# Optimization experiments

Measured on AMD Instinct MI355X. Metric: run time of the kernel, lower is better.

## Reference

```python
import jax, jax.numpy as jnp
from jax import lax
import numpy as np

H = 2048           # dec_units == encoder sequence length
LEAK = 0.2
EPS = 1e-5

def _leaky(x):
    return jnp.where(x >= 0, x, LEAK * x)

def _bn(x, g, b):
    # training-mode BatchNorm1d over (N, C, L): normalize per-channel over N and L
    m = x.mean(axis=(0, 2), keepdims=True)
    v = x.var(axis=(0, 2), keepdims=True)
    return (x - m) / jnp.sqrt(v + EPS) * g.reshape(1, -1, 1) + b.reshape(1, -1, 1)

def _conv(x, w, b):
    # x: (N, C, L), w: (O, I, K) -- valid conv, stride 1
    y = lax.conv_general_dilated(x, w, (1,), 'VALID', dimension_numbers=('NCH', 'OIH', 'NCH'))
    return y + b[None, :, None]

def setup_inputs() -> dict:
    key = jax.random.key(0)
    ks = jax.random.split(key, 40)
    def n(k, shape, s=0.05):
        return jax.random.normal(k, shape, dtype=jnp.float32) * s
    Lp = ((H - 20) // 2 - 8) // 2          # 503: conv/pool-reduced length
    inp = {
        'last_input': n(ks[0], (4,), 1.0),
        'hidden':     n(ks[1], (1, 1, H), 1.0),
        'enc_output': n(ks[2], (H, 1, 6), 1.0),
        'W1_w': n(ks[3], (H, 6)),   'W1_b': n(ks[4], (H,)),
        'W2_w': n(ks[5], (H, H)),   'W2_b': n(ks[6], (H,)),
        'V_w':  n(ks[7], (1, H + 1)), 'V_b': n(ks[8], (1,)),
        'bn1_g': 1.0 + n(ks[9], (1,)), 'bn1_b': n(ks[10], (1,)),
        'c1_w': n(ks[11], (6, 6, 11), 0.2), 'c1_b': n(ks[12], (6,)),
        'c2_w': n(ks[13], (6, 6, 11), 0.2), 'c2_b': n(ks[14], (6,)),
        'c3_w': n(ks[15], (6, 6, 5), 0.2),  'c3_b': n(ks[16], (6,)),
        'c4_w': n(ks[17], (6, 6, 5), 0.2),  'c4_b': n(ks[18], (6,)),
        'bn2_g': 1.0 + n(ks[19], (6,)), 'bn2_b': n(ks[20], (6,)),
        'gru_Wi': n(ks[21], (3 * H, 6), 0.2), 'gru_Wh': n(ks[22], (3 * H, H), 0.02),
        'gru_bi': n(ks[23], (3 * H,)),        'gru_bh': n(ks[24], (3 * H,)),
        'lin1_w': n(ks[25], (400, H), 0.02), 'lin1_b': n(ks[26], (400,)),
        'bn3_g': 1.0 + n(ks[27], (1,)), 'bn3_b': n(ks[28], (1,)),
        'lin2_w': n(ks[29], (1, 400)), 'lin2_b': n(ks[30], (1,)),
        'lin3_w': n(ks[31], (50, Lp + 4)), 'lin3_b': n(ks[32], (50,)),
        'lin4_w': n(ks[33], (4, 50)), 'lin4_b': n(ks[34], (4,)),
    }
    return inp

def _forward(last_input, hidden, enc_output, W1_w, W1_b, W2_w, W2_b, V_w, V_b,
             bn1_g, bn1_b, c1_w, c1_b, c2_w, c2_b, c3_w, c3_b, c4_w, c4_b,
             bn2_g, bn2_b, gru_Wi, gru_Wh, gru_bi, gru_bh,
             lin1_w, lin1_b, bn3_g, bn3_b, lin2_w, lin2_b, lin3_w, lin3_b, lin4_w, lin4_b):
    # --- Bahdanau-style attention score ---
    w1 = _leaky(enc_output @ W1_w.T + W1_b)                         # (H, 1, H)
    w2 = _leaky(jnp.transpose(hidden @ W2_w.T + W2_b, (2, 1, 0)))   # (H, 1, 1)
    cat = jnp.concatenate([w1, jnp.broadcast_to(w2, (H, 1, 1))], axis=-1)
    score = cat @ V_w.T + V_b                                       # (H, 1, 1)
    score = _leaky(_bn(score, bn1_g, bn1_b))
    weights = jax.nn.softmax(score, axis=0)
    context = jnp.transpose(enc_output * weights, (1, 2, 0))        # (1, 6, H)
    # --- small CNN feature extractor ---
    c = _leaky(_conv(context, c1_w, c1_b))
    c = _leaky(_conv(c, c2_w, c2_b))
    c = c.reshape(1, 6, -1, 2).max(axis=-1)                         # MaxPool1d(2)
    c = _leaky(_conv(c, c3_w, c3_b))
    c = _leaky(_conv(c, c4_w, c4_b))
    c = _bn(c, bn2_g, bn2_b)
    c = c.reshape(1, 6, -1, 2).max(axis=-1)                         # (1, 6, L')
    seq = jnp.transpose(c, (2, 0, 1))                               # (L', 1, 6)
    # --- GRU (torch gate order r, z, n) ---
    h0 = hidden[0]                                                  # (1, H)
    def step(h, x):
        gi = x @ gru_Wi.T + gru_bi
        gh = h @ gru_Wh.T + gru_bh
        ir, iz, inn = jnp.split(gi, 3, axis=-1)
        hr, hz, hn = jnp.split(gh, 3, axis=-1)
        r = jax.nn.sigmoid(ir + hr)
        z = jax.nn.sigmoid(iz + hz)
        ng = jnp.tanh(inn + r * hn)
        hn_new = (1.0 - z) * ng + z * h
        return hn_new, hn_new
    hT, xs = lax.scan(step, h0, seq)                                # xs: (L', 1, H)
    # --- MLP head (dropout = identity in eval) ---
    x = _leaky(xs)
    x = x @ lin1_w.T + lin1_b                                       # (L', 1, 400)
    x = _leaky(_bn(x, bn3_g, bn3_b))
    x = (x @ lin2_w.T + lin2_b).squeeze()                           # (L',)
    x = _leaky(x)
    x = jnp.concatenate([x, last_input])                            # (L'+4,)
    x = _leaky(x @ lin3_w.T + lin3_b)
    x = x @ lin4_w.T + lin4_b                                       # (4,)
    return x, hT[None]                                              # hidden: (1, 1, H)

def reference(last_input, hidden, enc_output, W1_w, W1_b, W2_w, W2_b, V_w, V_b,
              bn1_g, bn1_b, c1_w, c1_b, c2_w, c2_b, c3_w, c3_b, c4_w, c4_b,
              bn2_g, bn2_b, gru_Wi, gru_Wh, gru_bi, gru_bh,
              lin1_w, lin1_b, bn3_g, bn3_b, lin2_w, lin2_b, lin3_w, lin3_b, lin4_w, lin4_b):
    return _forward(last_input, hidden, enc_output, W1_w, W1_b, W2_w, W2_b, V_w, V_b,
                    bn1_g, bn1_b, c1_w, c1_b, c2_w, c2_b, c3_w, c3_b, c4_w, c4_b,
                    bn2_g, bn2_b, gru_Wi, gru_Wh, gru_bi, gru_bh,
                    lin1_w, lin1_b, bn3_g, bn3_b, lin2_w, lin2_b, lin3_w, lin3_b, lin4_w, lin4_b)
```

## Files before the change

### kernel.cpp

```cpp
#include <hip/hip_runtime.h>

#define LEAK 0.2f
#define EPS  1e-5f
#define TS   503
#define SCOPE_SYS __HIP_MEMORY_SCOPE_SYSTEM
typedef unsigned long long ull;

__device__ __forceinline__ float lrelu(float x){ return x >= 0.f ? x : LEAK * x; }

typedef _Float16 half2v __attribute__((ext_vector_type(2)));

__device__ __forceinline__ unsigned short f2h(float x){
  _Float16 h = (_Float16)x;
  return __builtin_bit_cast(unsigned short, h);
}

__device__ __forceinline__ float fdot2(unsigned a, unsigned b, float c){
#if __has_builtin(__builtin_amdgcn_fdot2)
  return __builtin_amdgcn_fdot2(__builtin_bit_cast(half2v, a),
                                __builtin_bit_cast(half2v, b), c, false);
#else
  half2v aa = __builtin_bit_cast(half2v, a);
  half2v bb = __builtin_bit_cast(half2v, b);
  return fmaf((float)aa[1], (float)bb[1], fmaf((float)aa[0], (float)bb[0], c));
#endif
}

template<bool MAXOP>
__device__ __forceinline__ float bred(float v, float* red){
  #pragma unroll
  for (int off = 32; off; off >>= 1){
    float o = __shfl_xor(v, off);
    v = MAXOP ? fmaxf(v, o) : (v + o);
  }
  int nw = blockDim.x >> 6;
  int wv = threadIdx.x >> 6, ln = threadIdx.x & 63;
  __syncthreads();
  if (ln == 0) red[wv] = v;
  __syncthreads();
  if (wv == 0){
    float x = (ln < nw) ? red[ln] : (MAXOP ? -3.402823466e38f : 0.f);
    #pragma unroll
    for (int off = 8; off; off >>= 1){
      float o = __shfl_xor(x, off);
      x = MAXOP ? fmaxf(x, o) : (x + o);
    }
    if (ln == 0) red[0] = x;
  }
  __syncthreads();
  return red[0];
}

__global__ void k_w2(const float* __restrict__ W2w, const float* __restrict__ W2b,
                     const float* __restrict__ hidden, float* __restrict__ w2v){
  int wave = threadIdx.x >> 6, lane = threadIdx.x & 63;
  int row = blockIdx.x*4 + wave;
  const float* wr = W2w + (size_t)row*2048;
  float acc = 0.f;
  #pragma unroll
  for (int k = 0; k < 8; ++k){
    int base = 4*lane + 256*k;
    float4 w = *(const float4*)(wr + base);
    float4 h = *(const float4*)(hidden + base);
    acc = fmaf(w.x,h.x, fmaf(w.y,h.y, fmaf(w.z,h.z, fmaf(w.w,h.w, acc))));
  }
  #pragma unroll
  for (int off = 32; off; off >>= 1) acc += __shfl_xor(acc, off);
  if (lane == 0) w2v[row] = lrelu(acc + W2b[row]);
}

__global__ void k_score(const float* __restrict__ enc, const float* __restrict__ W1w,
                        const float* __restrict__ W1b, const float* __restrict__ Vw,
                        const float* __restrict__ Vb, const float* __restrict__ w2v,
                        float* __restrict__ score){
  __shared__ float sW1[2048*6];
  int tid = threadIdx.x;
  for (int idx = tid; idx < 2048*6; idx += 256) sW1[idx] = W1w[idx];
  __syncthreads();
  int wave = tid >> 6, lane = tid & 63;
  int i = blockIdx.x*4 + wave;
  float e0 = enc[(size_t)i*6+0], e1 = enc[(size_t)i*6+1], e2 = enc[(size_t)i*6+2];
  float e3 = enc[(size_t)i*6+3], e4 = enc[(size_t)i*6+4], e5 = enc[(size_t)i*6+5];
  float acc = 0.f;
  for (int jj = 0; jj < 32; ++jj){
    int j = lane + 64*jj;
    const float* wr = sW1 + j*6;
    float a = fmaf(e0,wr[0], fmaf(e1,wr[1], fmaf(e2,wr[2],
              fmaf(e3,wr[3], fmaf(e4,wr[4], fmaf(e5,wr[5], W1b[j]))))));
    acc = fmaf(lrelu(a), Vw[j], acc);
  }
  #pragma unroll
  for (int off = 32; off; off >>= 1) acc += __shfl_xor(acc, off);
  if (lane == 0) score[i] = acc + w2v[i]*Vw[2048] + Vb[0];
}

__global__ void k_softctx(const float* __restrict__ enc, const float* __restrict__ score,
                          const float* g1, const float* b1, float* __restrict__ ctx){
  __shared__ float red[16];
  int tid = threadIdx.x;
  float s0 = score[tid], s1 = score[tid + 1024];
  float mean = bred<false>(s0 + s1, red) * (1.f/2048.f);
  float d0 = s0 - mean, d1 = s1 - mean;
  float var = bred<false>(d0*d0 + d1*d1, red) * (1.f/2048.f);
  float iv = rsqrtf(var + EPS);
  float g = g1[0], b = b1[0];
  float v0 = lrelu(d0*iv*g + b), v1 = lrelu(d1*iv*g + b);
  float mx = bred<true>(fmaxf(v0, v1), red);
  float e0 = expf(v0 - mx), e1 = expf(v1 - mx);
  float se = bred<false>(e0 + e1, red);
  float w0 = e0/se, w1 = e1/se;
  #pragma unroll
  for (int c = 0; c < 6; ++c){
    ctx[c*2048 + tid]        = enc[(size_t)tid*6 + c] * w0;
    ctx[c*2048 + tid + 1024] = enc[(size_t)(tid+1024)*6 + c] * w1;
  }
}

__global__ void k_conv(const float* __restrict__ in, int Lin,
                       float* __restrict__ out, int Lout,
                       const float* __restrict__ w, const float* __restrict__ b, int K){
  int idx = blockIdx.x*256 + threadIdx.x;
  if (idx >= 6*Lout) return;
  int o = idx / Lout, x = idx - o*Lout;
  float acc = b[o];
  for (int i = 0; i < 6; ++i){
    const float* ir = in + i*Lin + x;
    const float* wr = w + (o*6 + i)*K;
    for (int k = 0; k < K; ++k) acc = fmaf(ir[k], wr[k], acc);
  }
  out[o*Lout + x] = lrelu(acc);
}

__global__ void k_pool(const float* __restrict__ in, int Lin, float* __restrict__ out, int Lout){
  int idx = blockIdx.x*256 + threadIdx.x;
  if (idx >= 6*Lout) return;
  int o = idx / Lout, x = idx - o*Lout;
  out[idx] = fmaxf(in[o*Lin + 2*x], in[o*Lin + 2*x + 1]);
}

__global__ void k_bn2stats(const float* __restrict__ in, float* m6, float* i6){
  __shared__ float red[16];
  for (int c = 0; c < 6; ++c){
    float s = 0.f, s2 = 0.f;
    for (int i = threadIdx.x; i < 1006; i += 256){
      float v = in[c*1006 + i]; s += v; s2 += v*v;
    }
    s  = bred<false>(s, red);
    s2 = bred<false>(s2, red);
    if (threadIdx.x == 0){
      float m = s / 1006.f;
      float var = s2 / 1006.f - m*m;
      m6[c] = m; i6[c] = rsqrtf(var + EPS);
    }
  }
}

__global__ void k_seq(const float* __restrict__ cb4, const float* m6, const float* i6,
                      const float* g2, const float* b2, float* __restrict__ seq){
  int idx = blockIdx.x*256 + threadIdx.x;
  if (idx >= TS*6) return;
  int c = idx % 6, t = idx / 6;
  float m = m6[c], iv = i6[c], g = g2[c], b = b2[c];
  float v0 = (cb4[c*1006 + 2*t]     - m)*iv*g + b;
  float v1 = (cb4[c*1006 + 2*t + 1] - m)*iv*g + b;
  seq[idx] = fmaxf(v0, v1);
}

__global__ void k_gihat(const float* __restrict__ seq, const float* __restrict__ Wi,
                        const float* __restrict__ bi, float* __restrict__ gihat){
  int row = blockIdx.x*256 + threadIdx.x;
  int t = blockIdx.y;
  const float* s = seq + t*6;
  const float* w = Wi + (size_t)row*6;
  float v = fmaf(s[0],w[0], fmaf(s[1],w[1], fmaf(s[2],w[2],
            fmaf(s[3],w[3], fmaf(s[4],w[4], fmaf(s[5],w[5], bi[row]))))));
  gihat[(size_t)t*6144 + row] = v;
}

#define GRU_SMEM (24*2048*2 + 1024*4)

__global__ void __launch_bounds__(256, 1)
k_gru(const float* __restrict__ Wh, const float* __restrict__ bh,
      const float* __restrict__ hidden, const float* __restrict__ gihat,
      ull* hbuf, float* __restrict__ xs, float* __restrict__ dout){
  extern __shared__ char smem[];
  ushort* Wl    = (ushort*)smem;
  unsigned* h2  = (unsigned*)(smem + 24*2048*2);
  const int tid = threadIdx.x, wg = blockIdx.x;
  const int lane = tid & 63, w = tid >> 6;
  const int hbase = wg << 3;

  for (int idx = tid; idx < 24*2048; idx += 256){
    int lr = idx >> 11, col = idx & 2047;
    int wv = lr/6, k = lr - 6*wv, gate = k >> 1, o = k & 1;
    int grow = (gate << 11) + hbase + 2*wv + o;
    Wl[idx] = f2h(Wh[(size_t)grow*2048 + col]);
  }
  float bhr = 0.f, bhz = 0.f, bhn = 0.f, hold = 0.f;
  if (lane < 2){
    int o = hbase + 2*w + lane;
    bhr = bh[o]; bhz = bh[2048 + o]; bhn = bh[4096 + o];
    hold = hidden[o];
  }
  __syncthreads();

  for (int t = 0; t < TS; ++t){
    float gr = 0.f, gz = 0.f, gn = 0.f;
    if (lane < 2){
      const float* gp = gihat + (size_t)t*6144 + hbase + 2*w + lane;
      gr = gp[0]; gz = gp[2048]; gn = gp[4096];
    }
    if (t == 0){
      const float4* hp = (const float4*)(hidden + 8*tid);
      float4 a = hp[0], b = hp[1];
      unsigned p0 = (unsigned)f2h(a.x) | ((unsigned)f2h(a.y) << 16);
      unsigned p1 = (unsigned)f2h(a.z) | ((unsigned)f2h(a.w) << 16);
      unsigned p2 = (unsigned)f2h(b.x) | ((unsigned)f2h(b.y) << 16);
      unsigned p3 = (unsigned)f2h(b.z) | ((unsigned)f2h(b.w) << 16);
      *(uint4*)(h2 + 4*tid) = make_uint4(p0, p1, p2, p3);
    } else {
      const ull* src = hbuf + (size_t)((t - 1) & 1)*1024 + 4*tid;
      const unsigned expect = (unsigned)t;
      ull v[4];
      unsigned done = 0;
      for (;;){
        #pragma unroll
        for (int j = 0; j < 4; ++j)
          if (!((done >> j) & 1u))
            v[j] = __hip_atomic_load(src + j, __ATOMIC_RELAXED, SCOPE_SYS);
        unsigned nd = done;
        #pragma unroll
        for (int j = 0; j < 4; ++j)
          if ((unsigned)(v[j] >> 32) == expect) nd |= (1u << j);
        if (nd == 15u) break;
        done = nd;
        __builtin_amdgcn_s_sleep(1);
      }
      *(uint4*)(h2 + 4*tid) = make_uint4((unsigned)v[0], (unsigned)v[1],
                                         (unsigned)v[2], (unsigned)v[3]);
    }
    __syncthreads();

    uint4 hf[4];
    #pragma unroll
    for (int k = 0; k < 4; ++k)
      hf[k] = *(const uint4*)((const char*)h2 + 16*lane + 1024*k);
    float acc[6];
    #pragma unroll
    for (int rr = 0; rr < 6; ++rr){
      int lr = 6*w + rr;
      const char* wrow = (const char*)Wl + lr*4096 + 16*lane;
      float a = 0.f;
      #pragma unroll
      for (int k = 0; k < 4; ++k){
        uint4 wv = *(const uint4*)(wrow + 1024*k);
        a = fdot2(wv.x, hf[k].x, a);
        a = fdot2(wv.y, hf[k].y, a);
        a = fdot2(wv.z, hf[k].z, a);
        a = fdot2(wv.w, hf[k].w, a);
      }
      #pragma unroll
      for (int off = 32; off; off >>= 1) a += __shfl_xor(a, off);
      acc[rr] = a;
    }
    float hnew = 0.f;
    if (lane < 2){
      float r  = 1.f/(1.f + expf(-(gr + bhr + acc[0 + lane])));
      float z  = 1.f/(1.f + expf(-(gz + bhz + acc[2 + lane])));
      float ng = tanhf(gn + r*(acc[4 + lane] + bhn));
      hnew = (1.f - z)*ng + z*hold;
    }
    float hn1 = __shfl(hnew, 1);
    if (lane == 0){
      unsigned pair = (unsigned)f2h(hnew) | ((unsigned)f2h(hn1) << 16);
      ull pv = ((ull)(unsigned)(t + 1) << 32) | (ull)pair;
      __hip_atomic_store(hbuf + (size_t)(t & 1)*1024 + 4*wg + w, pv,
                         __ATOMIC_RELAXED, SCOPE_SYS);
    }
    if (lane < 2){
      xs[(size_t)t*2048 + hbase + 2*w + lane] = hnew;
      if (t == TS - 1) dout[4 + hbase + 2*w + lane] = hnew;
      hold = hnew;
    }
  }
}

__global__ void k_lin1(const float* __restrict__ xs, const float* __restrict__ W,
                       const float* __restrict__ B, float* __restrict__ y1){
  __shared__ float xT[32][36];
  __shared__ float wT[32][36];
  int tid = threadIdx.x;
  int m0 = blockIdx.y*32, n0 = blockIdx.x*32;
  int lm = tid >> 3, lk = (tid & 7)*4;
  int tx = tid & 15, ty = tid >> 4;
  float acc00=0.f, acc01=0.f, acc10=0.f, acc11=0.f;
  for (int k0 = 0; k0 < 2048; k0 += 32){
    float4 xv = make_float4(0.f,0.f,0.f,0.f);
    int tt = m0 + lm;
    if (tt < TS) xv = *(const float4*)(xs + (size_t)tt*2048 + k0 + lk);
    xT[lk+0][lm] = lrelu(xv.x); xT[lk+1][lm] = lrelu(xv.y);
    xT[lk+2][lm] = lrelu(xv.z); xT[lk+3][lm] = lrelu(xv.w);
    float4 wv = make_float4(0.f,0.f,0.f,0.f);
    int jj = n0 + lm;
    if (jj < 400) wv = *(const float4*)(W + (size_t)jj*2048 + k0 + lk);
    wT[lk+0][lm] = wv.x; wT[lk+1][lm] = wv.y; wT[lk+2][lm] = wv.z; wT[lk+3][lm] = wv.w;
    __syncthreads();
    #pragma unroll
    for (int k = 0; k < 32; ++k){
      float2 a = *(const float2*)&xT[k][2*ty];
      float2 b = *(const float2*)&wT[k][2*tx];
      acc00 = fmaf(a.x, b.x, acc00); acc01 = fmaf(a.x, b.y, acc01);
      acc10 = fmaf(a.y, b.x, acc10); acc11 = fmaf(a.y, b.y, acc11);
    }
    __syncthreads();
  }
  int t0 = m0 + 2*ty, j0 = n0 + 2*tx;
  if (t0 < TS){
    if (j0 < 400)   y1[t0*400 + j0]   = acc00 + B[j0];
    if (j0+1 < 400) y1[t0*400 + j0+1] = acc01 + B[j0+1];
  }
  if (t0+1 < TS){
    if (j0 < 400)   y1[(t0+1)*400 + j0]   = acc10 + B[j0];
    if (j0+1 < 400) y1[(t0+1)*400 + j0+1] = acc11 + B[j0+1];
  }
}

__global__ void k_bn3p(const float* __restrict__ y1, float* __restrict__ part){
  __shared__ float red[16];
  float s = 0.f, s2 = 0.f;
  for (int idx = blockIdx.x*256 + threadIdx.x; idx < TS*400; idx += 64*256){
    float v = y1[idx]; s += v; s2 += v*v;
  }
  s  = bred<false>(s, red);
  s2 = bred<false>(s2, red);
  if (threadIdx.x == 0){ part[blockIdx.x] = s; part[64 + blockIdx.x] = s2; }
}

__global__ void k_bn3f(const float* __restrict__ part, float* __restrict__ stats){
  int ln = threadIdx.x;
  float s = part[ln], s2 = part[64 + ln];
  #pragma unroll
  for (int off = 32; off; off >>= 1){ s += __shfl_xor(s, off); s2 += __shfl_xor(s2, off); }
  if (ln == 0){
    float m = s / (float)(TS*400);
    float var = s2 / (float)(TS*400) - m*m;
    stats[0] = m; stats[1] = rsqrtf(var + EPS);
  }
}

__global__ void k_x2(const float* __restrict__ y1, const float* __restrict__ stats,
                     const float* g3, const float* b3, const float* __restrict__ l2w,
                     const float* l2b, float* __restrict__ x2){
  int t = blockIdx.x, ln = threadIdx.x;
  float m = stats[0], iv = stats[1], g = g3[0], b = b3[0];
  float acc = 0.f;
  for (int j = ln; j < 400; j += 64)
    acc = fmaf(lrelu((y1[t*400 + j] - m)*iv*g + b), l2w[j], acc);
  #pragma unroll
  for (int off = 32; off; off >>= 1) acc += __shfl_xor(acc, off);
  if (ln == 0) x2[t] = lrelu(acc + l2b[0]);
}

__global__ void k_head(const float* __restrict__ x2, const float* __restrict__ last,
                       const float* __restrict__ l3w, const float* __restrict__ l3b,
                       const float* __restrict__ l4w, const float* __restrict__ l4b,
                       float* __restrict__ out){
  __shared__ float o1[50];
  int tid = threadIdx.x;
  if (tid < 50){
    float acc = l3b[tid];
    const float* wr = l3w + tid*507;
    for (int i = 0; i < TS; ++i) acc = fmaf(x2[i], wr[i], acc);
    for (int i = 0; i < 4; ++i)  acc = fmaf(last[i], wr[TS + i], acc);
    o1[tid] = lrelu(acc);
  }
  __syncthreads();
  if (tid < 4){
    float acc = l4b[tid];
    const float* wr = l4w + tid*50;
    for (int k = 0; k < 50; ++k) acc = fmaf(o1[k], wr[k], acc);
    out[tid] = acc;
  }
}

#define OFF_BN2M    1024u
#define OFF_BN2I    1056u
#define OFF_BN3P    2048u
#define OFF_BN3S    2560u
#define OFF_W2      4096u
#define OFF_SCORE   12288u
#define OFF_X2      20480u
#define OFF_CTX     24576u
#define OFF_CB1     73728u
#define OFF_HBUF    73728u
#define OFF_CB2     122880u
#define OFF_CP1     172032u
#define OFF_CB3     196608u
#define OFF_CB4     221184u
#define OFF_SEQ     245760u
#define OFF_GIHAT   274432u
#define OFF_XS      12636160u
#define OFF_Y1      16756736u

extern "C" void kernel_launch(void* const* d_in, const int* in_sizes, int n_in,
                              void* d_out, int out_size, void* d_ws, size_t ws_size,
                              hipStream_t stream){
  const float* last   = (const float*)d_in[0];
  const float* hidden = (const float*)d_in[1];
  const float* enc    = (const float*)d_in[2];
  const float* W1w = (const float*)d_in[3];
  const float* W1b = (const float*)d_in[4];
  const float* W2w = (const float*)d_in[5];
  const float* W2b = (const float*)d_in[6];
  const float* Vw  = (const float*)d_in[7];
  const float* Vb  = (const float*)d_in[8];
  const float* g1  = (const float*)d_in[9];
  const float* b1  = (const float*)d_in[10];
  const float* c1w = (const float*)d_in[11]; const float* c1b = (const float*)d_in[12];
  const float* c2w = (const float*)d_in[13]; const float* c2b = (const float*)d_in[14];
  const float* c3w = (const float*)d_in[15]; const float* c3b = (const float*)d_in[16];
  const float* c4w = (const float*)d_in[17]; const float* c4b = (const float*)d_in[18];
  const float* g2  = (const float*)d_in[19]; const float* b2  = (const float*)d_in[20];
  const float* Wi  = (const float*)d_in[21]; const float* Wh  = (const float*)d_in[22];
  const float* bi  = (const float*)d_in[23]; const float* bhp = (const float*)d_in[24];
  const float* l1w = (const float*)d_in[25]; const float* l1b = (const float*)d_in[26];
  const float* g3  = (const float*)d_in[27]; const float* b3  = (const float*)d_in[28];
  const float* l2w = (const float*)d_in[29]; const float* l2b = (const float*)d_in[30];
  const float* l3w = (const float*)d_in[31]; const float* l3b = (const float*)d_in[32];
  const float* l4w = (const float*)d_in[33]; const float* l4b = (const float*)d_in[34];
  float* out = (float*)d_out;
  char* ws = (char*)d_ws;

  float* bn2m  = (float*)(ws + OFF_BN2M);
  float* bn2i  = (float*)(ws + OFF_BN2I);
  float* bn3p  = (float*)(ws + OFF_BN3P);
  float* bn3s  = (float*)(ws + OFF_BN3S);
  float* w2v   = (float*)(ws + OFF_W2);
  float* score = (float*)(ws + OFF_SCORE);
  float* x2    = (float*)(ws + OFF_X2);
  float* ctx   = (float*)(ws + OFF_CTX);
  float* cb1   = (float*)(ws + OFF_CB1);
  ull*   hbuf  = (ull*)(ws + OFF_HBUF);
  float* cb2   = (float*)(ws + OFF_CB2);
  float* cp1   = (float*)(ws + OFF_CP1);
  float* cb3   = (float*)(ws + OFF_CB3);
  float* cb4   = (float*)(ws + OFF_CB4);
  float* seq   = (float*)(ws + OFF_SEQ);
  float* gihat = (float*)(ws + OFF_GIHAT);
  float* xs    = (float*)(ws + OFF_XS);
  float* y1    = (float*)(ws + OFF_Y1);

  k_w2<<<512, 256, 0, stream>>>(W2w, W2b, hidden, w2v);
  k_score<<<512, 256, 0, stream>>>(enc, W1w, W1b, Vw, Vb, w2v, score);
  k_softctx<<<1, 1024, 0, stream>>>(enc, score, g1, b1, ctx);

  k_conv<<<(6*2038 + 255)/256, 256, 0, stream>>>(ctx, 2048, cb1, 2038, c1w, c1b, 11);
  k_conv<<<(6*2028 + 255)/256, 256, 0, stream>>>(cb1, 2038, cb2, 2028, c2w, c2b, 11);
  hipMemsetAsync(hbuf, 0, 2*1024*sizeof(ull), stream);
  k_pool<<<(6*1014 + 255)/256, 256, 0, stream>>>(cb2, 2028, cp1, 1014);
  k_conv<<<(6*1010 + 255)/256, 256, 0, stream>>>(cp1, 1014, cb3, 1010, c3w, c3b, 5);
  k_conv<<<(6*1006 + 255)/256, 256, 0, stream>>>(cb3, 1010, cb4, 1006, c4w, c4b, 5);
  k_bn2stats<<<1, 256, 0, stream>>>(cb4, bn2m, bn2i);
  k_seq<<<12, 256, 0, stream>>>(cb4, bn2m, bn2i, g2, b2, seq);
  k_gihat<<<dim3(24, TS), 256, 0, stream>>>(seq, Wi, bi, gihat);

  hipFuncSetAttribute((const void*)k_gru, hipFuncAttributeMaxDynamicSharedMemorySize,
                      (int)GRU_SMEM);
  void* kargs[7] = {(void*)&Wh, (void*)&bhp, (void*)&hidden, (void*)&gihat,
                    (void*)&hbuf, (void*)&xs, (void*)&out};
  hipLaunchCooperativeKernel((const void*)k_gru, dim3(256), dim3(256), kargs,
                             (unsigned)GRU_SMEM, stream);

  k_lin1<<<dim3(13, 16), 256, 0, stream>>>(xs, l1w, l1b, y1);
  k_bn3p<<<64, 256, 0, stream>>>(y1, bn3p);
  k_bn3f<<<1, 64, 0, stream>>>(bn3p, bn3s);
  k_x2<<<TS, 64, 0, stream>>>(y1, bn3s, g3, b3, l2w, l2b, x2);
  k_head<<<1, 64, 0, stream>>>(x2, last, l3w, l3b, l4w, l4b, out);
}
```

Before: 2.465 ms.

## Add per-XCD leader relay for GRU hidden-state exchange

The cooperative GRU kernel now finds each workgroup's XCD through a hardware register and elects one leader workgroup per XCD. Only the leader polls the system-scope global hidden buffer; it copies each value into a per-XCD buffer at agent scope, and the other workgroups poll that local copy. Producers write to both buffers. The aim is to cut cross-die polling traffic and latency on the serial 503-step loop. The cost is an extra relay hop and extra stores, the sleep in the polling loop is removed, and the per-XCD buffer shares workspace space with y1, which is safe only because y1 is written after the GRU kernel finishes.

```diff
diff --git a/kernel.cpp b/kernel.cpp
--- a/kernel.cpp
+++ b/kernel.cpp
@@ -3,7 +3,8 @@
 #define LEAK 0.2f
 #define EPS  1e-5f
 #define TS   503
-#define SCOPE_SYS __HIP_MEMORY_SCOPE_SYSTEM
+#define SCOPE_AGENT __HIP_MEMORY_SCOPE_AGENT
+#define SCOPE_SYS   __HIP_MEMORY_SCOPE_SYSTEM
 typedef unsigned long long ull;
 
 __device__ __forceinline__ float lrelu(float x){ return x >= 0.f ? x : LEAK * x; }
@@ -177,18 +178,27 @@
   gihat[(size_t)t*6144 + row] = v;
 }
 
-#define GRU_SMEM (24*2048*2 + 1024*4)
+#define GRU_SMEM (24*2048*2 + 1024*4 + 16)
 
 __global__ void __launch_bounds__(256, 1)
 k_gru(const float* __restrict__ Wh, const float* __restrict__ bh,
       const float* __restrict__ hidden, const float* __restrict__ gihat,
-      ull* hbuf, float* __restrict__ xs, float* __restrict__ dout){
+      ull* hbuf, ull* xcdbuf, int* xcdrank,
+      float* __restrict__ xs, float* __restrict__ dout){
   extern __shared__ char smem[];
   ushort* Wl    = (ushort*)smem;
   unsigned* h2  = (unsigned*)(smem + 24*2048*2);
+  int* s_lead   = (int*)(smem + 24*2048*2 + 1024*4);
   const int tid = threadIdx.x, wg = blockIdx.x;
   const int lane = tid & 63, w = tid >> 6;
   const int hbase = wg << 3;
+
+  unsigned xcc;
+  asm volatile("s_getreg_b32 %0, hwreg(HW_REG_XCC_ID, 0, 4)" : "=s"(xcc));
+  if (tid == 0){
+    int r = __hip_atomic_fetch_add(xcdrank + xcc, 1, __ATOMIC_RELAXED, SCOPE_AGENT);
+    *s_lead = (r == 0) ? 1 : 0;
+  }
 
   for (int idx = tid; idx < 24*2048; idx += 256){
     int lr = idx >> 11, col = idx & 2047;
@@ -203,6 +213,8 @@
     hold = hidden[o];
   }
   __syncthreads();
+  const bool lead = (*s_lead != 0);
+  ull* lbuf = xcdbuf + (size_t)xcc * 2048;
 
   for (int t = 0; t < TS; ++t){
     float gr = 0.f, gz = 0.f, gn = 0.f;
@@ -219,22 +231,39 @@
       unsigned p3 = (unsigned)f2h(b.z) | ((unsigned)f2h(b.w) << 16);
       *(uint4*)(h2 + 4*tid) = make_uint4(p0, p1, p2, p3);
     } else {
-      const ull* src = hbuf + (size_t)((t - 1) & 1)*1024 + 4*tid;
+      const size_t pbase = (size_t)((t - 1) & 1) * 1024 + 4*tid;
       const unsigned expect = (unsigned)t;
       ull v[4];
       unsigned done = 0;
-      for (;;){
-        #pragma unroll
-        for (int j = 0; j < 4; ++j)
-          if (!((done >> j) & 1u))
-            v[j] = __hip_atomic_load(src + j, __ATOMIC_RELAXED, SCOPE_SYS);
-        unsigned nd = done;
-        #pragma unroll
-        for (int j = 0; j < 4; ++j)
-          if ((unsigned)(v[j] >> 32) == expect) nd |= (1u << j);
-        if (nd == 15u) break;
-        done = nd;
-        __builtin_amdgcn_s_sleep(1);
+      if (lead){
+        const ull* src = hbuf + pbase;
+        ull* dst = lbuf + pbase;
+        for (;;){
+          #pragma unroll
+          for (int j = 0; j < 4; ++j){
+            if (!((done >> j) & 1u)){
+              ull x = __hip_atomic_load(src + j, __ATOMIC_RELAXED, SCOPE_SYS);
+              if ((unsigned)(x >> 32) == expect){
+                v[j] = x;
+                __hip_atomic_store(dst + j, x, __ATOMIC_RELAXED, SCOPE_AGENT);
+                done |= (1u << j);
+              }
+            }
+          }
+          if (done == 15u) break;
+        }
+      } else {
+        const ull* src = lbuf + pbase;
+        for (;;){
+          #pragma unroll
+          for (int j = 0; j < 4; ++j){
+            if (!((done >> j) & 1u)){
+              ull x = __hip_atomic_load(src + j, __ATOMIC_RELAXED, SCOPE_AGENT);
+              if ((unsigned)(x >> 32) == expect){ v[j] = x; done |= (1u << j); }
+            }
+          }
+          if (done == 15u) break;
+        }
       }
       *(uint4*)(h2 + 4*tid) = make_uint4((unsigned)v[0], (unsigned)v[1],
                                          (unsigned)v[2], (unsigned)v[3]);
@@ -274,8 +303,9 @@
     if (lane == 0){
       unsigned pair = (unsigned)f2h(hnew) | ((unsigned)f2h(hn1) << 16);
       ull pv = ((ull)(unsigned)(t + 1) << 32) | (ull)pair;
-      __hip_atomic_store(hbuf + (size_t)(t & 1)*1024 + 4*wg + w, pv,
-                         __ATOMIC_RELAXED, SCOPE_SYS);
+      size_t slot = (size_t)(t & 1)*1024 + 4*wg + w;
+      __hip_atomic_store(hbuf + slot, pv, __ATOMIC_RELAXED, SCOPE_SYS);
+      __hip_atomic_store(lbuf + slot, pv, __ATOMIC_RELAXED, SCOPE_AGENT);
     }
     if (lane < 2){
       xs[(size_t)t*2048 + hbase + 2*w + lane] = hnew;
@@ -401,6 +431,8 @@
 #define OFF_GIHAT   274432u
 #define OFF_XS      12636160u
 #define OFF_Y1      16756736u
+#define OFF_XCDBUF  16756736u
+#define OFF_XCDRANK (16756736u + 131072u)
 
 extern "C" void kernel_launch(void* const* d_in, const int* in_sizes, int n_in,
                               void* d_out, int out_size, void* d_ws, size_t ws_size,
@@ -449,6 +481,8 @@
   float* gihat = (float*)(ws + OFF_GIHAT);
   float* xs    = (float*)(ws + OFF_XS);
   float* y1    = (float*)(ws + OFF_Y1);
+  ull*   xcdbuf  = (ull*)(ws + OFF_XCDBUF);
+  int*   xcdrank = (int*)(ws + OFF_XCDRANK);
 
   k_w2<<<512, 256, 0, stream>>>(W2w, W2b, hidden, w2v);
   k_score<<<512, 256, 0, stream>>>(enc, W1w, W1b, Vw, Vb, w2v, score);
@@ -457,6 +491,7 @@
   k_conv<<<(6*2038 + 255)/256, 256, 0, stream>>>(ctx, 2048, cb1, 2038, c1w, c1b, 11);
   k_conv<<<(6*2028 + 255)/256, 256, 0, stream>>>(cb1, 2038, cb2, 2028, c2w, c2b, 11);
   hipMemsetAsync(hbuf, 0, 2*1024*sizeof(ull), stream);
+  hipMemsetAsync(ws + OFF_XCDBUF, 0, 131072u + 128u, stream);
   k_pool<<<(6*1014 + 255)/256, 256, 0, stream>>>(cb2, 2028, cp1, 1014);
   k_conv<<<(6*1010 + 255)/256, 256, 0, stream>>>(cp1, 1014, cb3, 1010, c3w, c3b, 5);
   k_conv<<<(6*1006 + 255)/256, 256, 0, stream>>>(cb3, 1010, cb4, 1006, c4w, c4b, 5);
@@ -466,8 +501,9 @@
 
   hipFuncSetAttribute((const void*)k_gru, hipFuncAttributeMaxDynamicSharedMemorySize,
                       (int)GRU_SMEM);
-  void* kargs[7] = {(void*)&Wh, (void*)&bhp, (void*)&hidden, (void*)&gihat,
-                    (void*)&hbuf, (void*)&xs, (void*)&out};
+  void* kargs[9] = {(void*)&Wh, (void*)&bhp, (void*)&hidden, (void*)&gihat,
+                    (void*)&hbuf, (void*)&xcdbuf, (void*)&xcdrank,
+                    (void*)&xs, (void*)&out};
   hipLaunchCooperativeKernel((const void*)k_gru, dim3(256), dim3(256), kargs,
                              (unsigned)GRU_SMEM, stream);
 
```

After: 3.396 ms. 1.38x slower.

## Replace per-element tagged hidden-state polling with sharded arrival counters

Applied to the files above, without the earlier changes.

Each GRU step's cross-workgroup handoff used to poll 64-bit words carrying a step tag for every hidden pair. Now each workgroup publishes a plain 32-bit packed pair, drains its stores, and bumps one of 8 padded arrival counters. Waiters poll the 8 counters until every one reaches 32*t, then read the hidden vector once. This halves the exchanged data and cuts polling traffic, at the cost of an extra vmcnt drain, a barrier and an atomic add per step, plus reliance on relaxed atomics being ordered.

```diff
diff --git a/kernel.cpp b/kernel.cpp
--- a/kernel.cpp
+++ b/kernel.cpp
@@ -182,7 +182,7 @@
 __global__ void __launch_bounds__(256, 1)
 k_gru(const float* __restrict__ Wh, const float* __restrict__ bh,
       const float* __restrict__ hidden, const float* __restrict__ gihat,
-      ull* hbuf, float* __restrict__ xs, float* __restrict__ dout){
+      unsigned* hbuf, int* cnt, float* __restrict__ xs, float* __restrict__ dout){
   extern __shared__ char smem[];
   ushort* Wl    = (ushort*)smem;
   unsigned* h2  = (unsigned*)(smem + 24*2048*2);
@@ -219,25 +219,19 @@
       unsigned p3 = (unsigned)f2h(b.z) | ((unsigned)f2h(b.w) << 16);
       *(uint4*)(h2 + 4*tid) = make_uint4(p0, p1, p2, p3);
     } else {
-      const ull* src = hbuf + (size_t)((t - 1) & 1)*1024 + 4*tid;
-      const unsigned expect = (unsigned)t;
-      ull v[4];
-      unsigned done = 0;
+      const int target = 32*t;
       for (;;){
-        #pragma unroll
-        for (int j = 0; j < 4; ++j)
-          if (!((done >> j) & 1u))
-            v[j] = __hip_atomic_load(src + j, __ATOMIC_RELAXED, SCOPE_SYS);
-        unsigned nd = done;
-        #pragma unroll
-        for (int j = 0; j < 4; ++j)
-          if ((unsigned)(v[j] >> 32) == expect) nd |= (1u << j);
-        if (nd == 15u) break;
-        done = nd;
-        __builtin_amdgcn_s_sleep(1);
+        int c = 0;
+        if (lane < 8)
+          c = __hip_atomic_load(cnt + lane*16, __ATOMIC_RELAXED, SCOPE_SYS);
+        if (__all(lane >= 8 || c >= target)) break;
       }
-      *(uint4*)(h2 + 4*tid) = make_uint4((unsigned)v[0], (unsigned)v[1],
-                                         (unsigned)v[2], (unsigned)v[3]);
+      asm volatile("" ::: "memory");
+      const ull* src = (const ull*)hbuf + (size_t)((t - 1) & 1)*512 + 2*tid;
+      ull a = __hip_atomic_load(src,     __ATOMIC_RELAXED, SCOPE_SYS);
+      ull b = __hip_atomic_load(src + 1, __ATOMIC_RELAXED, SCOPE_SYS);
+      *(uint4*)(h2 + 4*tid) = make_uint4((unsigned)a, (unsigned)(a >> 32),
+                                         (unsigned)b, (unsigned)(b >> 32));
     }
     __syncthreads();
 
@@ -273,8 +267,7 @@
     float hn1 = __shfl(hnew, 1);
     if (lane == 0){
       unsigned pair = (unsigned)f2h(hnew) | ((unsigned)f2h(hn1) << 16);
-      ull pv = ((ull)(unsigned)(t + 1) << 32) | (ull)pair;
-      __hip_atomic_store(hbuf + (size_t)(t & 1)*1024 + 4*wg + w, pv,
+      __hip_atomic_store(hbuf + (size_t)(t & 1)*1024 + 4*wg + w, pair,
                          __ATOMIC_RELAXED, SCOPE_SYS);
     }
     if (lane < 2){
@@ -282,6 +275,10 @@
       if (t == TS - 1) dout[4 + hbase + 2*w + lane] = hnew;
       hold = hnew;
     }
+    asm volatile("s_waitcnt vmcnt(0)" ::: "memory");
+    __syncthreads();
+    if (tid == 0)
+      __hip_atomic_fetch_add(cnt + (wg & 7)*16, 1, __ATOMIC_RELAXED, SCOPE_SYS);
   }
 }
 
@@ -393,6 +390,7 @@
 #define OFF_CTX     24576u
 #define OFF_CB1     73728u
 #define OFF_HBUF    73728u
+#define OFF_CNT     81920u
 #define OFF_CB2     122880u
 #define OFF_CP1     172032u
 #define OFF_CB3     196608u
@@ -440,7 +438,8 @@
   float* x2    = (float*)(ws + OFF_X2);
   float* ctx   = (float*)(ws + OFF_CTX);
   float* cb1   = (float*)(ws + OFF_CB1);
-  ull*   hbuf  = (ull*)(ws + OFF_HBUF);
+  unsigned* hbuf = (unsigned*)(ws + OFF_HBUF);
+  int*   cnt   = (int*)(ws + OFF_CNT);
   float* cb2   = (float*)(ws + OFF_CB2);
   float* cp1   = (float*)(ws + OFF_CP1);
   float* cb3   = (float*)(ws + OFF_CB3);
@@ -456,7 +455,7 @@
 
   k_conv<<<(6*2038 + 255)/256, 256, 0, stream>>>(ctx, 2048, cb1, 2038, c1w, c1b, 11);
   k_conv<<<(6*2028 + 255)/256, 256, 0, stream>>>(cb1, 2038, cb2, 2028, c2w, c2b, 11);
-  hipMemsetAsync(hbuf, 0, 2*1024*sizeof(ull), stream);
+  hipMemsetAsync(ws + OFF_CNT, 0, 512, stream);
   k_pool<<<(6*1014 + 255)/256, 256, 0, stream>>>(cb2, 2028, cp1, 1014);
   k_conv<<<(6*1010 + 255)/256, 256, 0, stream>>>(cp1, 1014, cb3, 1010, c3w, c3b, 5);
   k_conv<<<(6*1006 + 255)/256, 256, 0, stream>>>(cb3, 1010, cb4, 1006, c4w, c4b, 5);
@@ -466,8 +465,8 @@
 
   hipFuncSetAttribute((const void*)k_gru, hipFuncAttributeMaxDynamicSharedMemorySize,
                       (int)GRU_SMEM);
-  void* kargs[7] = {(void*)&Wh, (void*)&bhp, (void*)&hidden, (void*)&gihat,
-                    (void*)&hbuf, (void*)&xs, (void*)&out};
+  void* kargs[8] = {(void*)&Wh, (void*)&bhp, (void*)&hidden, (void*)&gihat,
+                    (void*)&hbuf, (void*)&cnt, (void*)&xs, (void*)&out};
   hipLaunchCooperativeKernel((const void*)k_gru, dim3(256), dim3(256), kargs,
                              (unsigned)GRU_SMEM, stream);
 
```

Result: slower. 4.385 ms (+77.9%).

## Poll hidden state per wavefront into registers, drop LDS staging and barrier

Applied to the files above, without the earlier changes.

Each wavefront now polls all 16 hidden-state words it needs straight from the global flag buffer into registers, instead of each thread polling 4 words, staging them in LDS and hitting a workgroup barrier. To keep the dot products correct, the weight layout in LDS is permuted so each lane's contiguous hidden slice lines up with its weight chunks. This removes the per-step __syncthreads and the LDS round trip on the GRU critical path. In exchange, every wavefront issues four times as many system-scope atomic loads per step, and exit now waits on a wave-wide __all vote.

```diff
diff --git a/kernel.cpp b/kernel.cpp
--- a/kernel.cpp
+++ b/kernel.cpp
@@ -13,6 +13,10 @@
 __device__ __forceinline__ unsigned short f2h(float x){
   _Float16 h = (_Float16)x;
   return __builtin_bit_cast(unsigned short, h);
+}
+
+__device__ __forceinline__ unsigned packh2(float a, float b){
+  return (unsigned)f2h(a) | ((unsigned)f2h(b) << 16);
 }
 
 __device__ __forceinline__ float fdot2(unsigned a, unsigned b, float c){
@@ -177,22 +181,23 @@
   gihat[(size_t)t*6144 + row] = v;
 }
 
-#define GRU_SMEM (24*2048*2 + 1024*4)
+#define GRU_SMEM (24*2048*2)
 
 __global__ void __launch_bounds__(256, 1)
 k_gru(const float* __restrict__ Wh, const float* __restrict__ bh,
       const float* __restrict__ hidden, const float* __restrict__ gihat,
       ull* hbuf, float* __restrict__ xs, float* __restrict__ dout){
   extern __shared__ char smem[];
-  ushort* Wl    = (ushort*)smem;
-  unsigned* h2  = (unsigned*)(smem + 24*2048*2);
+  ushort* Wl = (ushort*)smem;
   const int tid = threadIdx.x, wg = blockIdx.x;
   const int lane = tid & 63, w = tid >> 6;
   const int hbase = wg << 3;
 
   for (int idx = tid; idx < 24*2048; idx += 256){
-    int lr = idx >> 11, col = idx & 2047;
-    int wv = lr/6, k = lr - 6*wv, gate = k >> 1, o = k & 1;
+    int lr = idx >> 11, q = idx & 2047;
+    int k = q >> 9, i = (q >> 3) & 63, e = q & 7;
+    int col = 32*i + 8*k + e;
+    int wv = lr/6, kk = lr - 6*wv, gate = kk >> 1, o = kk & 1;
     int grow = (gate << 11) + hbase + 2*wv + o;
     Wl[idx] = f2h(Wh[(size_t)grow*2048 + col]);
   }
@@ -204,6 +209,7 @@
   }
   __syncthreads();
 
+  uint4 hf[4];
   for (int t = 0; t < TS; ++t){
     float gr = 0.f, gz = 0.f, gn = 0.f;
     if (lane < 2){
@@ -211,40 +217,37 @@
       gr = gp[0]; gz = gp[2048]; gn = gp[4096];
     }
     if (t == 0){
-      const float4* hp = (const float4*)(hidden + 8*tid);
-      float4 a = hp[0], b = hp[1];
-      unsigned p0 = (unsigned)f2h(a.x) | ((unsigned)f2h(a.y) << 16);
-      unsigned p1 = (unsigned)f2h(a.z) | ((unsigned)f2h(a.w) << 16);
-      unsigned p2 = (unsigned)f2h(b.x) | ((unsigned)f2h(b.y) << 16);
-      unsigned p3 = (unsigned)f2h(b.z) | ((unsigned)f2h(b.w) << 16);
-      *(uint4*)(h2 + 4*tid) = make_uint4(p0, p1, p2, p3);
+      const float* hp = hidden + 32*lane;
+      #pragma unroll
+      for (int k = 0; k < 4; ++k){
+        float4 a = *(const float4*)(hp + 8*k);
+        float4 b = *(const float4*)(hp + 8*k + 4);
+        hf[k] = make_uint4(packh2(a.x, a.y), packh2(a.z, a.w),
+                           packh2(b.x, b.y), packh2(b.z, b.w));
+      }
     } else {
-      const ull* src = hbuf + (size_t)((t - 1) & 1)*1024 + 4*tid;
+      const ull* src = hbuf + (size_t)((t - 1) & 1)*1024 + 16*lane;
       const unsigned expect = (unsigned)t;
-      ull v[4];
       unsigned done = 0;
       for (;;){
+        ull v[16];
         #pragma unroll
-        for (int j = 0; j < 4; ++j)
+        for (int j = 0; j < 16; ++j)
           if (!((done >> j) & 1u))
             v[j] = __hip_atomic_load(src + j, __ATOMIC_RELAXED, SCOPE_SYS);
         unsigned nd = done;
         #pragma unroll
-        for (int j = 0; j < 4; ++j)
-          if ((unsigned)(v[j] >> 32) == expect) nd |= (1u << j);
-        if (nd == 15u) break;
+        for (int j = 0; j < 16; ++j)
+          if (!((done >> j) & 1u) && (unsigned)(v[j] >> 32) == expect){
+            nd |= (1u << j);
+            ((unsigned*)hf)[j] = (unsigned)v[j];
+          }
+        if (__all(nd == 0xFFFFu)){ break; }
         done = nd;
         __builtin_amdgcn_s_sleep(1);
       }
-      *(uint4*)(h2 + 4*tid) = make_uint4((unsigned)v[0], (unsigned)v[1],
-                                         (unsigned)v[2], (unsigned)v[3]);
-    }
-    __syncthreads();
-
-    uint4 hf[4];
-    #pragma unroll
-    for (int k = 0; k < 4; ++k)
-      hf[k] = *(const uint4*)((const char*)h2 + 16*lane + 1024*k);
+    }
+
     float acc[6];
     #pragma unroll
     for (int rr = 0; rr < 6; ++rr){
@@ -253,11 +256,11 @@
       float a = 0.f;
       #pragma unroll
       for (int k = 0; k < 4; ++k){
-        uint4 wv = *(const uint4*)(wrow + 1024*k);
-        a = fdot2(wv.x, hf[k].x, a);
-        a = fdot2(wv.y, hf[k].y, a);
-        a = fdot2(wv.z, hf[k].z, a);
-        a = fdot2(wv.w, hf[k].w, a);
+        uint4 wv4 = *(const uint4*)(wrow + (k << 10));
+        a = fdot2(wv4.x, hf[k].x, a);
+        a = fdot2(wv4.y, hf[k].y, a);
+        a = fdot2(wv4.z, hf[k].z, a);
+        a = fdot2(wv4.w, hf[k].w, a);
       }
       #pragma unroll
       for (int off = 32; off; off >>= 1) a += __shfl_xor(a, off);
@@ -272,8 +275,7 @@
     }
     float hn1 = __shfl(hnew, 1);
     if (lane == 0){
-      unsigned pair = (unsigned)f2h(hnew) | ((unsigned)f2h(hn1) << 16);
-      ull pv = ((ull)(unsigned)(t + 1) << 32) | (ull)pair;
+      ull pv = ((ull)(unsigned)(t + 1) << 32) | (ull)packh2(hnew, hn1);
       __hip_atomic_store(hbuf + (size_t)(t & 1)*1024 + 4*wg + w, pv,
                          __ATOMIC_RELAXED, SCOPE_SYS);
     }
```

New measurement: 5.324 ms. 2.16x slower.
